# Kernel optimization log

Measured on AMD Instinct MI355X. Metric: run time of the kernel, lower is better.

Reference implementation:

```python
import math
import jax, jax.numpy as jnp
import numpy as np

IN_CH = 512
KEY = 512
VAL = 512
B, T = 8, 2048
SQRT_KEY = math.sqrt(float(KEY))


def setup_inputs() -> dict:
    key = jax.random.key(0)
    ks = jax.random.split(key, 7)
    s_in = 1.0 / math.sqrt(IN_CH)
    return {
        "x": jax.random.normal(ks[0], (B, T, IN_CH), dtype=jnp.float32),
        "Wq": jax.random.uniform(ks[1], (IN_CH, KEY), jnp.float32, -s_in, s_in),
        "bq": jax.random.uniform(ks[2], (KEY,), jnp.float32, -s_in, s_in),
        "Wk": jax.random.uniform(ks[3], (IN_CH, KEY), jnp.float32, -s_in, s_in),
        "bk": jax.random.uniform(ks[4], (KEY,), jnp.float32, -s_in, s_in),
        "Wv": jax.random.uniform(ks[5], (IN_CH, VAL), jnp.float32, -s_in, s_in),
        "bv": jax.random.uniform(ks[6], (VAL,), jnp.float32, -s_in, s_in),
    }


def reference(x, Wq, bq, Wk, bk, Wv, bv):
    # x: [B, T, C]
    q = x @ Wq + bq          # [B, T, K]
    k = x @ Wk + bk          # [B, T, K]
    v = x @ Wv + bv          # [B, T, V]
    logits = jnp.einsum("btk,bsk->bts", q, k)  # [B, T(q), T(kv)]
    mask = jnp.tril(jnp.ones((T, T), dtype=bool))  # causal: key s <= query t
    logits = jnp.where(mask[None, :, :], logits, -jnp.inf)
    # NOTE: original torch code softmaxes over dim=1 (the QUERY axis) — kept faithful.
    probs = jax.nn.softmax(logits / SQRT_KEY, axis=1)
    read = jnp.einsum("bts,bsv->btv", probs, v)  # [B, T, V]
    return jnp.concatenate((x, read), axis=2)    # [B, T, C+V]
```

## Files before the change

kernel.cpp:

```cpp
#include <hip/hip_runtime.h>
#include <hip/hip_bf16.h>
#include <math.h>

#define BATCH 8
#define SEQ   2048
#define CH    512
#define ROWS  (BATCH * SEQ)
#define INVSQ 0.044194173824159216f

#define BM 128
#define BK 32
#define TILE_ELEMS (BM * BK)
#define TP 68

typedef __attribute__((ext_vector_type(8))) __bf16 bf16x8;
typedef __attribute__((ext_vector_type(4))) float f32x4;

__device__ inline unsigned short f2bf(float f) {
    unsigned u = __builtin_bit_cast(unsigned, f);
    u += 0x7fffu + ((u >> 16) & 1u);
    return (unsigned short)(u >> 16);
}
__device__ inline float bf2f(unsigned short s) {
    unsigned u = ((unsigned)s) << 16;
    return __builtin_bit_cast(float, u);
}

__device__ __forceinline__ void stage_tile(
    const unsigned short* __restrict__ gbase, size_t stride,
    unsigned short* lds, int wave, int lane)
{
#pragma unroll
    for (int j = 0; j < 2; ++j) {
        int chunk = wave * 2 + j;
        int row = chunk * 16 + (lane >> 2);
        const unsigned short* g = gbase + (size_t)row * stride + ((lane & 3) << 3);
        __builtin_amdgcn_global_load_lds(
            (const __attribute__((address_space(1))) unsigned int*)g,
            (__attribute__((address_space(3))) unsigned int*)(lds + (chunk << 9)),
            16, 0, 0);
    }
}

__device__ __forceinline__ void load_frags(
    const unsigned short* lds, int w0, int l16, int quad, bf16x8* f)
{
#pragma unroll
    for (int r = 0; r < 4; ++r)
        f[r] = *(const bf16x8*)(lds + (w0 + r * 16 + l16) * BK + quad * 8);
}

__global__ __launch_bounds__(256) void fuse_x_kernel(
    const float* __restrict__ x, unsigned short* __restrict__ xb,
    float* __restrict__ out, float* __restrict__ Z)
{
    if (blockIdx.x < 64) Z[blockIdx.x * 256 + threadIdx.x] = 0.f;
    size_t base = ((size_t)blockIdx.x * 256 + threadIdx.x) * 8;
    size_t row = base >> 9, c = base & 511;
    float4 v0 = *(const float4*)(x + base);
    float4 v1 = *(const float4*)(x + base + 4);
    float* o = out + row * 1024 + c;
    *(float4*)o = v0;
    *(float4*)(o + 4) = v1;
    alignas(16) unsigned short t[8];
    t[0] = f2bf(v0.x); t[1] = f2bf(v0.y); t[2] = f2bf(v0.z); t[3] = f2bf(v0.w);
    t[4] = f2bf(v1.x); t[5] = f2bf(v1.y); t[6] = f2bf(v1.z); t[7] = f2bf(v1.w);
    *(uint4*)(xb + base) = *(const uint4*)t;
}

__global__ __launch_bounds__(256) void transpose_w_kernel(
    const float* __restrict__ Wq, const float* __restrict__ Wk,
    const float* __restrict__ Wv, unsigned short* __restrict__ Wt)
{
    __shared__ unsigned short T[64 * TP];
    const int k0 = blockIdx.x * 64, n0 = blockIdx.y * 64, w = blockIdx.z;
    const float* W = (w == 0) ? Wq : (w == 1) ? Wk : Wv;
    const int tid = threadIdx.x;
#pragma unroll
    for (int i = 0; i < 2; ++i) {
        int slot = tid + i * 256;
        int kr = slot >> 3, c8 = (slot & 7) << 3;
        float4 a = *(const float4*)(W + (size_t)(k0 + kr) * CH + n0 + c8);
        float4 b = *(const float4*)(W + (size_t)(k0 + kr) * CH + n0 + c8 + 4);
        T[(c8 + 0) * TP + kr] = f2bf(a.x); T[(c8 + 1) * TP + kr] = f2bf(a.y);
        T[(c8 + 2) * TP + kr] = f2bf(a.z); T[(c8 + 3) * TP + kr] = f2bf(a.w);
        T[(c8 + 4) * TP + kr] = f2bf(b.x); T[(c8 + 5) * TP + kr] = f2bf(b.y);
        T[(c8 + 6) * TP + kr] = f2bf(b.z); T[(c8 + 7) * TP + kr] = f2bf(b.w);
    }
    __syncthreads();
#pragma unroll
    for (int i = 0; i < 2; ++i) {
        int slot = tid + i * 256;
        int nr = slot >> 3, k8 = (slot & 7) << 3;
        uint2 lo = *(const uint2*)(T + nr * TP + k8);
        uint2 hi = *(const uint2*)(T + nr * TP + k8 + 4);
        uint4 u; u.x = lo.x; u.y = lo.y; u.z = hi.x; u.w = hi.y;
        *(uint4*)(Wt + ((size_t)w * CH + n0 + nr) * CH + k0 + k8) = u;
    }
}

__global__ __launch_bounds__(256) void transpose_v_kernel(
    const unsigned short* __restrict__ vb, const float* __restrict__ Z,
    unsigned short* __restrict__ Vt)
{
    __shared__ unsigned short T[64 * TP];
    const int s0 = blockIdx.x * 64, v0 = blockIdx.y * 64, b = blockIdx.z;
    const int tid = threadIdx.x;
#pragma unroll
    for (int i = 0; i < 2; ++i) {
        int slot = tid + i * 256;
        int sr = slot >> 3, c8 = (slot & 7) << 3;
        float inv = 1.0f / Z[b * SEQ + s0 + sr];
        uint4 raw = *(const uint4*)(vb + ((size_t)b * SEQ + s0 + sr) * CH + v0 + c8);
        const unsigned short* p = (const unsigned short*)&raw;
#pragma unroll
        for (int j = 0; j < 8; ++j)
            T[(c8 + j) * TP + sr] = f2bf(bf2f(p[j]) * inv);
    }
    __syncthreads();
#pragma unroll
    for (int i = 0; i < 2; ++i) {
        int slot = tid + i * 256;
        int vr = slot >> 3, s8 = (slot & 7) << 3;
        uint2 lo = *(const uint2*)(T + vr * TP + s8);
        uint2 hi = *(const uint2*)(T + vr * TP + s8 + 4);
        uint4 u; u.x = lo.x; u.y = lo.y; u.z = hi.x; u.w = hi.y;
        *(uint4*)(Vt + ((size_t)b * CH + v0 + vr) * SEQ + s0 + s8) = u;
    }
}

__global__ __launch_bounds__(256) void qkv_kernel(
    const unsigned short* __restrict__ xb, const unsigned short* __restrict__ Wt,
    const float* __restrict__ bq, const float* __restrict__ bk,
    const float* __restrict__ bv, unsigned short* __restrict__ qkv)
{
    __shared__ unsigned short As[2 * TILE_ELEMS];
    __shared__ unsigned short Bs[2 * TILE_ELEMS];
    const int xrow0 = blockIdx.x * BM;
    const int wrow0 = blockIdx.y * BM;
    const int tid = threadIdx.x;
    const int lane = tid & 63, wave = tid >> 6;
    const int wm = (wave >> 1) * 64, wn = (wave & 1) * 64;
    const int quad = lane >> 4, l16 = lane & 15;

    f32x4 acc[4][4] = {};
    for (int kk = 0; kk < CH; kk += 64) {
        stage_tile(Wt + (size_t)wrow0 * CH + kk,      CH, As,              wave, lane);
        stage_tile(Wt + (size_t)wrow0 * CH + kk + 32, CH, As + TILE_ELEMS, wave, lane);
        stage_tile(xb + (size_t)xrow0 * CH + kk,      CH, Bs,              wave, lane);
        stage_tile(xb + (size_t)xrow0 * CH + kk + 32, CH, Bs + TILE_ELEMS, wave, lane);
        __syncthreads();
#pragma unroll
        for (int h = 0; h < 2; ++h) {
            bf16x8 a[4], bb[4];
            load_frags(As + h * TILE_ELEMS, wm, l16, quad, a);
            load_frags(Bs + h * TILE_ELEMS, wn, l16, quad, bb);
#pragma unroll
            for (int r = 0; r < 4; ++r)
#pragma unroll
                for (int c = 0; c < 4; ++c)
                    acc[r][c] = __builtin_amdgcn_mfma_f32_16x16x32_bf16(a[r], bb[c], acc[r][c], 0, 0, 0);
        }
        __syncthreads();
    }
    const int which = wrow0 >> 9;
    const float* bias = (which == 0) ? bq : (which == 1) ? bk : bv;
    const float scale = (which == 0) ? INVSQ : 1.0f;
    unsigned short* outw = qkv + (size_t)which * ROWS * CH;
    const int colblk = wrow0 & 511;
#pragma unroll
    for (int r = 0; r < 4; ++r) {
        int colb = colblk + wm + r * 16 + quad * 4;
        float4 b4 = *(const float4*)(bias + colb);
#pragma unroll
        for (int c = 0; c < 4; ++c) {
            int m = xrow0 + wn + c * 16 + l16;
            alignas(8) unsigned short pk[4];
            pk[0] = f2bf((acc[r][c][0] + b4.x) * scale);
            pk[1] = f2bf((acc[r][c][1] + b4.y) * scale);
            pk[2] = f2bf((acc[r][c][2] + b4.z) * scale);
            pk[3] = f2bf((acc[r][c][3] + b4.w) * scale);
            *(uint2*)(outw + (size_t)m * CH + colb) = *(const uint2*)pk;
        }
    }
}

__global__ __launch_bounds__(256) void logits_kernel(
    const unsigned short* __restrict__ qb, const unsigned short* __restrict__ kb,
    unsigned short* __restrict__ E, float* __restrict__ Z)
{
    __shared__ unsigned short As[2 * TILE_ELEMS];
    __shared__ unsigned short Bs[2 * TILE_ELEMS];
    const int id = blockIdx.x;
    const int b = id & 7;
    const int i = id >> 3;
    int tt = (int)((sqrtf(8.f * (float)i + 1.f) - 1.f) * 0.5f);
    int st = i - ((tt * (tt + 1)) >> 1);
    while (st < 0)  { --tt; st = i - ((tt * (tt + 1)) >> 1); }
    while (st > tt) { ++tt; st = i - ((tt * (tt + 1)) >> 1); }
    const int m0s = st * BM;
    const int n0t = tt * BM;
    const int tid = threadIdx.x;
    const int lane = tid & 63, wave = tid >> 6;
    const int wm = (wave >> 1) * 64, wn = (wave & 1) * 64;
    const int quad = lane >> 4, l16 = lane & 15;
    const unsigned short* kB = kb + (size_t)b * SEQ * CH;
    const unsigned short* qB = qb + (size_t)b * SEQ * CH;

    f32x4 acc[4][4] = {};
    for (int kk = 0; kk < CH; kk += 64) {
        stage_tile(kB + (size_t)m0s * CH + kk,      CH, As,              wave, lane);
        stage_tile(kB + (size_t)m0s * CH + kk + 32, CH, As + TILE_ELEMS, wave, lane);
        stage_tile(qB + (size_t)n0t * CH + kk,      CH, Bs,              wave, lane);
        stage_tile(qB + (size_t)n0t * CH + kk + 32, CH, Bs + TILE_ELEMS, wave, lane);
        __syncthreads();
#pragma unroll
        for (int h = 0; h < 2; ++h) {
            bf16x8 a[4], bb[4];
            load_frags(As + h * TILE_ELEMS, wm, l16, quad, a);
            load_frags(Bs + h * TILE_ELEMS, wn, l16, quad, bb);
#pragma unroll
            for (int r = 0; r < 4; ++r)
#pragma unroll
                for (int c = 0; c < 4; ++c)
                    acc[r][c] = __builtin_amdgcn_mfma_f32_16x16x32_bf16(a[r], bb[c], acc[r][c], 0, 0, 0);
        }
        __syncthreads();
    }
#pragma unroll
    for (int r = 0; r < 4; ++r) {
        int sb = m0s + wm + r * 16 + quad * 4;
        float ev[4][4];
#pragma unroll
        for (int c = 0; c < 4; ++c) {
            int t = n0t + wn + c * 16 + l16;
#pragma unroll
            for (int reg = 0; reg < 4; ++reg)
                ev[c][reg] = (sb + reg <= t) ? __expf(acc[r][c][reg]) : 0.f;
        }
#pragma unroll
        for (int reg = 0; reg < 4; ++reg) {
            float z = ev[0][reg] + ev[1][reg] + ev[2][reg] + ev[3][reg];
            z += __shfl_xor(z, 1);
            z += __shfl_xor(z, 2);
            z += __shfl_xor(z, 4);
            z += __shfl_xor(z, 8);
            if (l16 == 0) atomicAdd(&Z[b * SEQ + sb + reg], z);
        }
#pragma unroll
        for (int c = 0; c < 4; ++c) {
            int t = n0t + wn + c * 16 + l16;
            alignas(8) unsigned short pk[4];
            pk[0] = f2bf(ev[c][0]); pk[1] = f2bf(ev[c][1]);
            pk[2] = f2bf(ev[c][2]); pk[3] = f2bf(ev[c][3]);
            *(uint2*)(E + ((size_t)b * SEQ + t) * SEQ + sb) = *(const uint2*)pk;
        }
    }
}

__global__ __launch_bounds__(256) void read_kernel(
    const unsigned short* __restrict__ E, const unsigned short* __restrict__ Vt,
    float* __restrict__ out)
{
    __shared__ unsigned short As[2 * TILE_ELEMS];
    __shared__ unsigned short Bs[2 * TILE_ELEMS];
    const int id = blockIdx.x;
    const int b = id & 7;
    const int rem = id >> 3;
    const int mv = rem & 3;
    const int r0 = rem >> 2;
    const int tt = (r0 < 8) ? r0 : 23 - r0;
    const int m0v = mv * BM;
    const int n0t = tt * BM;
    const int Kmax = (tt + 1) * BM;
    const int tid = threadIdx.x;
    const int lane = tid & 63, wave = tid >> 6;
    const int wm = (wave >> 1) * 64, wn = (wave & 1) * 64;
    const int quad = lane >> 4, l16 = lane & 15;
    const unsigned short* Vb = Vt + (size_t)b * CH * SEQ;
    const unsigned short* Eb = E + (size_t)b * SEQ * SEQ;

    f32x4 acc[4][4] = {};
    for (int kk = 0; kk < Kmax; kk += 64) {
        stage_tile(Vb + (size_t)m0v * SEQ + kk,      SEQ, As,              wave, lane);
        stage_tile(Vb + (size_t)m0v * SEQ + kk + 32, SEQ, As + TILE_ELEMS, wave, lane);
        stage_tile(Eb + (size_t)n0t * SEQ + kk,      SEQ, Bs,              wave, lane);
        stage_tile(Eb + (size_t)n0t * SEQ + kk + 32, SEQ, Bs + TILE_ELEMS, wave, lane);
        __syncthreads();
#pragma unroll
        for (int h = 0; h < 2; ++h) {
            bf16x8 a[4], bb[4];
            load_frags(As + h * TILE_ELEMS, wm, l16, quad, a);
            load_frags(Bs + h * TILE_ELEMS, wn, l16, quad, bb);
#pragma unroll
            for (int r = 0; r < 4; ++r)
#pragma unroll
                for (int c = 0; c < 4; ++c)
                    acc[r][c] = __builtin_amdgcn_mfma_f32_16x16x32_bf16(a[r], bb[c], acc[r][c], 0, 0, 0);
        }
        __syncthreads();
    }
#pragma unroll
    for (int r = 0; r < 4; ++r) {
        int v = 512 + m0v + wm + r * 16 + quad * 4;
#pragma unroll
        for (int c = 0; c < 4; ++c) {
            int t = n0t + wn + c * 16 + l16;
            float4 f;
            f.x = acc[r][c][0]; f.y = acc[r][c][1];
            f.z = acc[r][c][2]; f.w = acc[r][c][3];
            *(float4*)(out + ((size_t)b * SEQ + t) * 1024 + v) = f;
        }
    }
}

extern "C" void kernel_launch(void* const* d_in, const int* in_sizes, int n_in,
                              void* d_out, int out_size, void* d_ws, size_t ws_size,
                              hipStream_t stream) {
    const float* x  = (const float*)d_in[0];
    const float* Wq = (const float*)d_in[1];
    const float* bq = (const float*)d_in[2];
    const float* Wk = (const float*)d_in[3];
    const float* bk = (const float*)d_in[4];
    const float* Wv = (const float*)d_in[5];
    const float* bv = (const float*)d_in[6];
    float* out = (float*)d_out;

    char* ws = (char*)d_ws;
    const size_t QKV_BYTES = (size_t)ROWS * CH * 2;
    const size_t E_BYTES   = (size_t)BATCH * SEQ * SEQ * 2;
    unsigned short* qkv = (unsigned short*)ws;
    unsigned short* qb = qkv;
    unsigned short* kb = (unsigned short*)(ws + QKV_BYTES);
    unsigned short* vb = (unsigned short*)(ws + 2 * QKV_BYTES);
    unsigned short* E  = (unsigned short*)(ws + 3 * QKV_BYTES);
    float* Z = (float*)(ws + 3 * QKV_BYTES + E_BYTES);
    unsigned short* xb = E;
    unsigned short* Wt = (unsigned short*)((char*)E + QKV_BYTES);
    unsigned short* Vt = qb;

    dim3 blk(256);
    fuse_x_kernel<<<dim3(4096), blk, 0, stream>>>(x, xb, out, Z);
    transpose_w_kernel<<<dim3(8, 8, 3), blk, 0, stream>>>(Wq, Wk, Wv, Wt);
    qkv_kernel<<<dim3(128, 12), blk, 0, stream>>>(xb, Wt, bq, bk, bv, qkv);
    logits_kernel<<<dim3(1088), blk, 0, stream>>>(qb, kb, E, Z);
    transpose_v_kernel<<<dim3(32, 8, 8), blk, 0, stream>>>(vb, Z, Vt);
    read_kernel<<<dim3(512), blk, 0, stream>>>(E, Vt, out);
}
```

Baseline: 238.2 us.

## Switch GEMM kernels to 32x32x16 MFMA tiles with precomputed staging pointers

```diff
diff --git a/kernel.cpp b/kernel.cpp
--- a/kernel.cpp
+++ b/kernel.cpp
@@ -9,12 +9,11 @@
 #define INVSQ 0.044194173824159216f
 
 #define BM 128
-#define BK 32
-#define TILE_ELEMS (BM * BK)
+#define TILE_ELEMS (BM * 32)
 #define TP 68
 
 typedef __attribute__((ext_vector_type(8))) __bf16 bf16x8;
-typedef __attribute__((ext_vector_type(4))) float f32x4;
+typedef __attribute__((ext_vector_type(16))) float f32x16;
 
 __device__ inline unsigned short f2bf(float f) {
     unsigned u = __builtin_bit_cast(unsigned, f);
@@ -26,28 +25,61 @@
     return __builtin_bit_cast(float, u);
 }
 
-__device__ __forceinline__ void stage_tile(
-    const unsigned short* __restrict__ gbase, size_t stride,
-    unsigned short* lds, int wave, int lane)
-{
-#pragma unroll
-    for (int j = 0; j < 2; ++j) {
-        int chunk = wave * 2 + j;
-        int row = chunk * 16 + (lane >> 2);
-        const unsigned short* g = gbase + (size_t)row * stride + ((lane & 3) << 3);
-        __builtin_amdgcn_global_load_lds(
-            (const __attribute__((address_space(1))) unsigned int*)g,
-            (__attribute__((address_space(3))) unsigned int*)(lds + (chunk << 9)),
-            16, 0, 0);
-    }
-}
-
-__device__ __forceinline__ void load_frags(
-    const unsigned short* lds, int w0, int l16, int quad, bf16x8* f)
-{
-#pragma unroll
-    for (int r = 0; r < 4; ++r)
-        f[r] = *(const bf16x8*)(lds + (w0 + r * 16 + l16) * BK + quad * 8);
+struct Stager {
+    const unsigned short* p[4];
+    unsigned short* d[4];
+    __device__ __forceinline__ void init(
+        const unsigned short* gbase, size_t stride,
+        unsigned short* lds, int wave, int lane)
+    {
+        int r = lane >> 2, c = (lane & 3) << 3;
+#pragma unroll
+        for (int h = 0; h < 2; ++h)
+#pragma unroll
+            for (int j = 0; j < 2; ++j) {
+                int chunk = wave * 2 + j;
+                p[h * 2 + j] = gbase + (size_t)(chunk * 16 + r) * stride + h * 32 + c;
+                d[h * 2 + j] = lds + h * TILE_ELEMS + (chunk << 9);
+            }
+    }
+    __device__ __forceinline__ void issue() {
+#pragma unroll
+        for (int i = 0; i < 4; ++i)
+            __builtin_amdgcn_global_load_lds(
+                (const __attribute__((address_space(1))) unsigned int*)p[i],
+                (__attribute__((address_space(3))) unsigned int*)d[i], 16, 0, 0);
+    }
+    __device__ __forceinline__ void advance() {
+#pragma unroll
+        for (int i = 0; i < 4; ++i) p[i] += 64;
+    }
+};
+
+__device__ __forceinline__ void compute_step(
+    const unsigned short* As, const unsigned short* Bs,
+    int wm, int wn, int l31, int h5, f32x16 acc[2][2])
+{
+#pragma unroll
+    for (int hbuf = 0; hbuf < 2; ++hbuf) {
+        const unsigned short* Ab = As + hbuf * TILE_ELEMS;
+        const unsigned short* Bb = Bs + hbuf * TILE_ELEMS;
+#pragma unroll
+        for (int j = 0; j < 2; ++j) {
+            bf16x8 a[2], bb[2];
+#pragma unroll
+            for (int mi = 0; mi < 2; ++mi)
+                a[mi] = *(const bf16x8*)(Ab + (wm + mi * 32 + l31) * 32 + j * 16 + h5 * 8);
+#pragma unroll
+            for (int ni = 0; ni < 2; ++ni)
+                bb[ni] = *(const bf16x8*)(Bb + (wn + ni * 32 + l31) * 32 + j * 16 + h5 * 8);
+#pragma unroll
+            for (int mi = 0; mi < 2; ++mi)
+#pragma unroll
+                for (int ni = 0; ni < 2; ++ni)
+                    acc[mi][ni] = __builtin_amdgcn_mfma_f32_32x32x16_bf16(
+                        a[mi], bb[ni], acc[mi][ni], 0, 0, 0);
+        }
+    }
 }
 
 __global__ __launch_bounds__(256) void fuse_x_kernel(
@@ -141,27 +173,20 @@
     const int tid = threadIdx.x;
     const int lane = tid & 63, wave = tid >> 6;
     const int wm = (wave >> 1) * 64, wn = (wave & 1) * 64;
-    const int quad = lane >> 4, l16 = lane & 15;
-
-    f32x4 acc[4][4] = {};
-    for (int kk = 0; kk < CH; kk += 64) {
-        stage_tile(Wt + (size_t)wrow0 * CH + kk,      CH, As,              wave, lane);
-        stage_tile(Wt + (size_t)wrow0 * CH + kk + 32, CH, As + TILE_ELEMS, wave, lane);
-        stage_tile(xb + (size_t)xrow0 * CH + kk,      CH, Bs,              wave, lane);
-        stage_tile(xb + (size_t)xrow0 * CH + kk + 32, CH, Bs + TILE_ELEMS, wave, lane);
-        __syncthreads();
-#pragma unroll
-        for (int h = 0; h < 2; ++h) {
-            bf16x8 a[4], bb[4];
-            load_frags(As + h * TILE_ELEMS, wm, l16, quad, a);
-            load_frags(Bs + h * TILE_ELEMS, wn, l16, quad, bb);
-#pragma unroll
-            for (int r = 0; r < 4; ++r)
-#pragma unroll
-                for (int c = 0; c < 4; ++c)
-                    acc[r][c] = __builtin_amdgcn_mfma_f32_16x16x32_bf16(a[r], bb[c], acc[r][c], 0, 0, 0);
-        }
-        __syncthreads();
+    const int l31 = lane & 31, h5 = lane >> 5;
+
+    Stager sA, sB;
+    sA.init(Wt + (size_t)wrow0 * CH, CH, As, wave, lane);
+    sB.init(xb + (size_t)xrow0 * CH, CH, Bs, wave, lane);
+
+    f32x16 acc[2][2] = {};
+#pragma unroll
+    for (int ks = 0; ks < CH / 64; ++ks) {
+        sA.issue(); sB.issue();
+        __syncthreads();
+        compute_step(As, Bs, wm, wn, l31, h5, acc);
+        __syncthreads();
+        sA.advance(); sB.advance();
     }
     const int which = wrow0 >> 9;
     const float* bias = (which == 0) ? bq : (which == 1) ? bk : bv;
@@ -169,20 +194,22 @@
     unsigned short* outw = qkv + (size_t)which * ROWS * CH;
     const int colblk = wrow0 & 511;
 #pragma unroll
-    for (int r = 0; r < 4; ++r) {
-        int colb = colblk + wm + r * 16 + quad * 4;
-        float4 b4 = *(const float4*)(bias + colb);
-#pragma unroll
-        for (int c = 0; c < 4; ++c) {
-            int m = xrow0 + wn + c * 16 + l16;
-            alignas(8) unsigned short pk[4];
-            pk[0] = f2bf((acc[r][c][0] + b4.x) * scale);
-            pk[1] = f2bf((acc[r][c][1] + b4.y) * scale);
-            pk[2] = f2bf((acc[r][c][2] + b4.z) * scale);
-            pk[3] = f2bf((acc[r][c][3] + b4.w) * scale);
-            *(uint2*)(outw + (size_t)m * CH + colb) = *(const uint2*)pk;
+    for (int mi = 0; mi < 2; ++mi)
+#pragma unroll
+        for (int rj = 0; rj < 4; ++rj) {
+            int colb = colblk + wm + mi * 32 + rj * 8 + h5 * 4;
+            float4 b4 = *(const float4*)(bias + colb);
+#pragma unroll
+            for (int ni = 0; ni < 2; ++ni) {
+                int m = xrow0 + wn + ni * 32 + l31;
+                alignas(8) unsigned short pk[4];
+                pk[0] = f2bf((acc[mi][ni][rj * 4 + 0] + b4.x) * scale);
+                pk[1] = f2bf((acc[mi][ni][rj * 4 + 1] + b4.y) * scale);
+                pk[2] = f2bf((acc[mi][ni][rj * 4 + 2] + b4.z) * scale);
+                pk[3] = f2bf((acc[mi][ni][rj * 4 + 3] + b4.w) * scale);
+                *(uint2*)(outw + (size_t)m * CH + colb) = *(const uint2*)pk;
+            }
         }
-    }
 }
 
 __global__ __launch_bounds__(256) void logits_kernel(
@@ -203,59 +230,53 @@
     const int tid = threadIdx.x;
     const int lane = tid & 63, wave = tid >> 6;
     const int wm = (wave >> 1) * 64, wn = (wave & 1) * 64;
-    const int quad = lane >> 4, l16 = lane & 15;
-    const unsigned short* kB = kb + (size_t)b * SEQ * CH;
-    const unsigned short* qB = qb + (size_t)b * SEQ * CH;
-
-    f32x4 acc[4][4] = {};
-    for (int kk = 0; kk < CH; kk += 64) {
-        stage_tile(kB + (size_t)m0s * CH + kk,      CH, As,              wave, lane);
-        stage_tile(kB + (size_t)m0s * CH + kk + 32, CH, As + TILE_ELEMS, wave, lane);
-        stage_tile(qB + (size_t)n0t * CH + kk,      CH, Bs,              wave, lane);
-        stage_tile(qB + (size_t)n0t * CH + kk + 32, CH, Bs + TILE_ELEMS, wave, lane);
-        __syncthreads();
-#pragma unroll
-        for (int h = 0; h < 2; ++h) {
-            bf16x8 a[4], bb[4];
-            load_frags(As + h * TILE_ELEMS, wm, l16, quad, a);
-            load_frags(Bs + h * TILE_ELEMS, wn, l16, quad, bb);
-#pragma unroll
-            for (int r = 0; r < 4; ++r)
-#pragma unroll
-                for (int c = 0; c < 4; ++c)
-                    acc[r][c] = __builtin_amdgcn_mfma_f32_16x16x32_bf16(a[r], bb[c], acc[r][c], 0, 0, 0);
+    const int l31 = lane & 31, h5 = lane >> 5;
+
+    Stager sA, sB;
+    sA.init(kb + (size_t)b * SEQ * CH + (size_t)m0s * CH, CH, As, wave, lane);
+    sB.init(qb + (size_t)b * SEQ * CH + (size_t)n0t * CH, CH, Bs, wave, lane);
+
+    f32x16 acc[2][2] = {};
+#pragma unroll
+    for (int ks = 0; ks < CH / 64; ++ks) {
+        sA.issue(); sB.issue();
+        __syncthreads();
+        compute_step(As, Bs, wm, wn, l31, h5, acc);
+        __syncthreads();
+        sA.advance(); sB.advance();
+    }
+#pragma unroll
+    for (int mi = 0; mi < 2; ++mi)
+#pragma unroll
+        for (int rj = 0; rj < 4; ++rj) {
+            int sb = m0s + wm + mi * 32 + rj * 8 + h5 * 4;
+            float ev[2][4];
+#pragma unroll
+            for (int ni = 0; ni < 2; ++ni) {
+                int t = n0t + wn + ni * 32 + l31;
+#pragma unroll
+                for (int ri = 0; ri < 4; ++ri)
+                    ev[ni][ri] = (sb + ri <= t) ? __expf(acc[mi][ni][rj * 4 + ri]) : 0.f;
+            }
+#pragma unroll
+            for (int ri = 0; ri < 4; ++ri) {
+                float z = ev[0][ri] + ev[1][ri];
+                z += __shfl_xor(z, 1);
+                z += __shfl_xor(z, 2);
+                z += __shfl_xor(z, 4);
+                z += __shfl_xor(z, 8);
+                z += __shfl_xor(z, 16);
+                if (l31 == 0) atomicAdd(&Z[b * SEQ + sb + ri], z);
+            }
+#pragma unroll
+            for (int ni = 0; ni < 2; ++ni) {
+                int t = n0t + wn + ni * 32 + l31;
+                alignas(8) unsigned short pk[4];
+                pk[0] = f2bf(ev[ni][0]); pk[1] = f2bf(ev[ni][1]);
+                pk[2] = f2bf(ev[ni][2]); pk[3] = f2bf(ev[ni][3]);
+                *(uint2*)(E + ((size_t)b * SEQ + t) * SEQ + sb) = *(const uint2*)pk;
+            }
         }
-        __syncthreads();
-    }
-#pragma unroll
-    for (int r = 0; r < 4; ++r) {
-        int sb = m0s + wm + r * 16 + quad * 4;
-        float ev[4][4];
-#pragma unroll
-        for (int c = 0; c < 4; ++c) {
-            int t = n0t + wn + c * 16 + l16;
-#pragma unroll
-            for (int reg = 0; reg < 4; ++reg)
-                ev[c][reg] = (sb + reg <= t) ? __expf(acc[r][c][reg]) : 0.f;
-        }
-#pragma unroll
-        for (int reg = 0; reg < 4; ++reg) {
-            float z = ev[0][reg] + ev[1][reg] + ev[2][reg] + ev[3][reg];
-            z += __shfl_xor(z, 1);
-            z += __shfl_xor(z, 2);
-            z += __shfl_xor(z, 4);
-            z += __shfl_xor(z, 8);
-            if (l16 == 0) atomicAdd(&Z[b * SEQ + sb + reg], z);
-        }
-#pragma unroll
-        for (int c = 0; c < 4; ++c) {
-            int t = n0t + wn + c * 16 + l16;
-            alignas(8) unsigned short pk[4];
-            pk[0] = f2bf(ev[c][0]); pk[1] = f2bf(ev[c][1]);
-            pk[2] = f2bf(ev[c][2]); pk[3] = f2bf(ev[c][3]);
-            *(uint2*)(E + ((size_t)b * SEQ + t) * SEQ + sb) = *(const uint2*)pk;
-        }
-    }
 }
 
 __global__ __launch_bounds__(256) void read_kernel(
@@ -272,46 +293,38 @@
     const int tt = (r0 < 8) ? r0 : 23 - r0;
     const int m0v = mv * BM;
     const int n0t = tt * BM;
-    const int Kmax = (tt + 1) * BM;
+    const int nsteps = ((tt + 1) * BM) / 64;
     const int tid = threadIdx.x;
     const int lane = tid & 63, wave = tid >> 6;
     const int wm = (wave >> 1) * 64, wn = (wave & 1) * 64;
-    const int quad = lane >> 4, l16 = lane & 15;
-    const unsigned short* Vb = Vt + (size_t)b * CH * SEQ;
-    const unsigned short* Eb = E + (size_t)b * SEQ * SEQ;
-
-    f32x4 acc[4][4] = {};
-    for (int kk = 0; kk < Kmax; kk += 64) {
-        stage_tile(Vb + (size_t)m0v * SEQ + kk,      SEQ, As,              wave, lane);
-        stage_tile(Vb + (size_t)m0v * SEQ + kk + 32, SEQ, As + TILE_ELEMS, wave, lane);
-        stage_tile(Eb + (size_t)n0t * SEQ + kk,      SEQ, Bs,              wave, lane);
-        stage_tile(Eb + (size_t)n0t * SEQ + kk + 32, SEQ, Bs + TILE_ELEMS, wave, lane);
-        __syncthreads();
-#pragma unroll
-        for (int h = 0; h < 2; ++h) {
-            bf16x8 a[4], bb[4];
-            load_frags(As + h * TILE_ELEMS, wm, l16, quad, a);
-            load_frags(Bs + h * TILE_ELEMS, wn, l16, quad, bb);
-#pragma unroll
-            for (int r = 0; r < 4; ++r)
-#pragma unroll
-                for (int c = 0; c < 4; ++c)
-                    acc[r][c] = __builtin_amdgcn_mfma_f32_16x16x32_bf16(a[r], bb[c], acc[r][c], 0, 0, 0);
+    const int l31 = lane & 31, h5 = lane >> 5;
+
+    Stager sA, sB;
+    sA.init(Vt + (size_t)b * CH * SEQ + (size_t)m0v * SEQ, SEQ, As, wave, lane);
+    sB.init(E + (size_t)b * SEQ * SEQ + (size_t)n0t * SEQ, SEQ, Bs, wave, lane);
+
+    f32x16 acc[2][2] = {};
+    for (int ks = 0; ks < nsteps; ++ks) {
+        sA.issue(); sB.issue();
+        __syncthreads();
+        compute_step(As, Bs, wm, wn, l31, h5, acc);
+        __syncthreads();
+        sA.advance(); sB.advance();
+    }
+#pragma unroll
+    for (int mi = 0; mi < 2; ++mi)
+#pragma unroll
+        for (int rj = 0; rj < 4; ++rj) {
+            int v = 512 + m0v + wm + mi * 32 + rj * 8 + h5 * 4;
+#pragma unroll
+            for (int ni = 0; ni < 2; ++ni) {
+                int t = n0t + wn + ni * 32 + l31;
+                float4 f;
+                f.x = acc[mi][ni][rj * 4 + 0]; f.y = acc[mi][ni][rj * 4 + 1];
+                f.z = acc[mi][ni][rj * 4 + 2]; f.w = acc[mi][ni][rj * 4 + 3];
+                *(float4*)(out + ((size_t)b * SEQ + t) * 1024 + v) = f;
+            }
         }
-        __syncthreads();
-    }
-#pragma unroll
-    for (int r = 0; r < 4; ++r) {
-        int v = 512 + m0v + wm + r * 16 + quad * 4;
-#pragma unroll
-        for (int c = 0; c < 4; ++c) {
-            int t = n0t + wn + c * 16 + l16;
-            float4 f;
-            f.x = acc[r][c][0]; f.y = acc[r][c][1];
-            f.z = acc[r][c][2]; f.w = acc[r][c][3];
-            *(float4*)(out + ((size_t)b * SEQ + t) * 1024 + v) = f;
-        }
-    }
 }
 
 extern "C" void kernel_launch(void* const* d_in, const int* in_sizes, int n_in,
```

Result: slower. 246.4 us (+3.5%).
